# Optimization experiments

Hardware: AMD Instinct MI355X
Metric: run time of the kernel (lower is better)

Reference implementation:

```python
import jax, jax.numpy as jnp
import numpy as np
import math

B, S, D, H = 8, 512, 768, 12
DK = D // H
NEG = 1.0e9


def _split_heads(x):
    # [B,S,D] -> [B,H,S,DK]
    b, s, d = x.shape
    return x.reshape(b, s, H, DK).transpose(0, 2, 1, 3)


def setup_inputs() -> dict:
    key = jax.random.key(0)
    ks = jax.random.split(key, 16)
    std = 1.0 / math.sqrt(D)
    query = jax.random.normal(ks[0], (B, S, D), jnp.float32)
    key_t = jax.random.normal(ks[1], (B, S, D), jnp.float32)
    # mask: 0 for valid tokens, -10000 sentinel for padding
    mask = jnp.where(jax.random.bernoulli(ks[2], 0.9, (B, S)), 0.0, -10000.0).astype(jnp.float32)
    # span targets: binary [H,B,S,S]
    span_matrix = jax.random.bernoulli(ks[3], 0.1, (H, B, S, S)).astype(jnp.float32)
    def lin(i):
        W = jax.random.normal(ks[4 + 2 * i], (D, D), jnp.float32) * std
        b = jax.random.normal(ks[5 + 2 * i], (D,), jnp.float32) * std
        return W, b
    Wql, bql = lin(0)
    Wkl, bkl = lin(1)
    Wqr, bqr = lin(2)
    Wkr, bkr = lin(3)
    Wq, bq = lin(4)
    Wk, bk = lin(5)
    return dict(query=query, key=key_t, mask=mask, span_matrix=span_matrix,
                Wql=Wql, bql=bql, Wkl=Wkl, bkl=bkl,
                Wqr=Wqr, bqr=bqr, Wkr=Wkr, bkr=bkr,
                Wq=Wq, bq=bq, Wk=Wk, bk=bk)


def _forward(query, key, mask, span_matrix,
             Wql, bql, Wkl, bkl, Wqr, bqr, Wkr, bkr, Wq, bq, Wk, bk):
    scale = 1.0 / math.sqrt(D)  # note: original scales by sqrt(model_dim), not sqrt(d_k)
    idx = jnp.arange(S)
    lower = idx[None, :] <= idx[:, None]  # [S,S] lower-triangular incl. diag
    left_boundary = jnp.where(lower, 0.0, NEG)   # 1e9 above diagonal
    right_boundary = left_boundary.T             # 1e9 below diagonal

    # left branch
    ql = _split_heads(query @ Wql + bql) * scale
    kl = _split_heads(key @ Wkl + bkl)
    left_scores = jnp.einsum('bhqd,bhkd->bhqk', ql, kl)
    theta_l = jax.nn.softmax(left_scores - left_boundary, axis=-1)

    # right branch
    qr = _split_heads(query @ Wqr + bqr) * scale
    kr = _split_heads(key @ Wkr + bkr)
    right_scores = jnp.einsum('bhqd,bhkd->bhqk', qr, kr)
    theta_r = jax.nn.softmax(right_scores - right_boundary, axis=-1)

    # theta_l @ upperTri == inclusive cumsum over last axis (O(S) instead of O(S^2) matmul)
    soft_Mask_l = jnp.cumsum(theta_l, axis=-1)
    # theta_r @ lowerTri == inclusive reverse cumsum over last axis
    soft_Mask_r = jnp.cumsum(theta_r[..., ::-1], axis=-1)[..., ::-1]
    soft_Mask = soft_Mask_l * soft_Mask_r

    # main attention
    q = _split_heads(query @ Wq + bq) * scale
    k = _split_heads(key @ Wk + bk)
    att_scores = jnp.einsum('bhqd,bhkd->bhqk', q, k)
    row_mask = jnp.where(mask == -10000.0, NEG, mask)  # [B,S]
    att_scores = att_scores - row_mask[:, None, :, None] - row_mask[:, None, None, :]
    p_local_attn = jax.nn.softmax(att_scores * soft_Mask, axis=-1)

    # per-head BCE between sigmoid(attn) and span targets; mean over heads of per-head means
    # == global mean since every head has the same element count
    span = span_matrix.transpose(1, 0, 2, 3)  # [B,H,S,S]
    p_sig = jax.nn.sigmoid(p_local_attn)      # in (0.5, 0.732], logs are safe
    bce = -(span * jnp.log(p_sig) + (1.0 - span) * jnp.log1p(-p_sig))
    span_loss = jnp.mean(bce)
    return p_local_attn, span_loss


def reference(query, key, mask, span_matrix,
              Wql, bql, Wkl, bkl, Wqr, bqr, Wkr, bkr, Wq, bq, Wk, bk):
    return _forward(query, key, mask, span_matrix,
                    Wql, bql, Wkl, bkl, Wqr, bqr, Wkr, bkr, Wq, bq, Wk, bk)
```

## Files before the change

### kernel.cpp

```cpp
#include <hip/hip_runtime.h>
#include <math.h>

#define BB 8
#define SS 512
#define DD 768
#define HH 12
#define DKK 64
#define NTOK (BB*SS)
#define NELEM (25165824ull)
#define NPROJ 3145728
#define WSZ   589824
#define SCALEQ 0.03608439182435161f

typedef unsigned short u16;
typedef short short8 __attribute__((ext_vector_type(8)));
typedef float f32x4 __attribute__((ext_vector_type(4)));
typedef unsigned short u16x4 __attribute__((ext_vector_type(4)));

#define MFMA16 __builtin_amdgcn_mfma_f32_16x16x32_bf16

__device__ inline u16 f32_to_bf16(float f) {
    unsigned int u = __float_as_uint(f);
    unsigned int r = u + 0x7fffu + ((u >> 16) & 1u);
    return (u16)(r >> 16);
}
__device__ inline float bf16_to_f32(u16 h) {
    return __uint_as_float(((unsigned int)h) << 16);
}

__device__ __forceinline__ void gld16(const u16* g, u16* l) {
    __builtin_amdgcn_global_load_lds(
        (const __attribute__((address_space(1))) unsigned int*)g,
        (__attribute__((address_space(3))) unsigned int*)l, 16, 0, 0);
}

__global__ __launch_bounds__(256)
void cast_wT(const float* __restrict__ W0, const float* __restrict__ W1,
             const float* __restrict__ W2, const float* __restrict__ W3,
             const float* __restrict__ W4, const float* __restrict__ W5,
             u16* __restrict__ WTh, u16* __restrict__ WTl,
             float* __restrict__ lossp)
{
    __shared__ float tile[32][33];
    if (blockIdx.x == 0 && blockIdx.y == 0 && blockIdx.z == 0 && threadIdx.x == 0)
        *lossp = 0.0f;
    const int z = blockIdx.z;
    const float* W;
    switch (z) {
        case 0: W = W0; break; case 1: W = W1; break; case 2: W = W2; break;
        case 3: W = W3; break; case 4: W = W4; break; default: W = W5; break;
    }
    u16* th = WTh + (size_t)z * WSZ;
    u16* tl = WTl + (size_t)z * WSZ;
    const int t = threadIdx.x;
    const int k0 = blockIdx.y * 32, n0 = blockIdx.x * 32;
    const int rr = t >> 3, c0 = (t & 7) * 4;

    float4 v = *(const float4*)(W + (size_t)(k0 + rr) * DD + n0 + c0);
    tile[rr][c0 + 0] = v.x; tile[rr][c0 + 1] = v.y;
    tile[rr][c0 + 2] = v.z; tile[rr][c0 + 3] = v.w;
    __syncthreads();

    u16x4 hw, lw;
#pragma unroll
    for (int i = 0; i < 4; ++i) {
        float f = tile[c0 + i][rr];
        u16 hi = f32_to_bf16(f);
        hw[i] = hi;
        lw[i] = f32_to_bf16(f - bf16_to_f32(hi));
    }
    size_t o = (size_t)(n0 + rr) * DD + k0 + c0;
    *(u16x4*)&th[o] = hw;
    *(u16x4*)&tl[o] = lw;
}

__global__ __launch_bounds__(256)
void cast_X(const float* __restrict__ query, const float* __restrict__ key,
            u16* __restrict__ Xh, u16* __restrict__ Xl)
{
    const float* src = blockIdx.y ? key : query;
    u16* dh = Xh + (size_t)blockIdx.y * NPROJ;
    u16* dl = Xl + (size_t)blockIdx.y * NPROJ;
    size_t i0 = ((size_t)blockIdx.x * 256 + threadIdx.x) * 8;
    float f[8];
    *(float4*)&f[0] = *(const float4*)(src + i0);
    *(float4*)&f[4] = *(const float4*)(src + i0 + 4);
    short8 h, l;
#pragma unroll
    for (int i = 0; i < 8; ++i) {
        u16 hi = f32_to_bf16(f[i]);
        h[i] = (short)hi;
        l[i] = (short)f32_to_bf16(f[i] - bf16_to_f32(hi));
    }
    *(short8*)&dh[i0] = h;
    *(short8*)&dl[i0] = l;
}

__global__ __launch_bounds__(256)
void proj_gemm_gld(const u16* __restrict__ Xh, const u16* __restrict__ Xl,
                   const u16* __restrict__ WTh, const u16* __restrict__ WTl,
                   const float* __restrict__ b0, const float* __restrict__ b1,
                   const float* __restrict__ b2, const float* __restrict__ b3,
                   const float* __restrict__ b4, const float* __restrict__ b5,
                   u16* __restrict__ Ph, u16* __restrict__ Pl)
{
    __shared__ alignas(16) u16 Ash[128][32];
    __shared__ alignas(16) u16 Asl[128][32];
    __shared__ alignas(16) u16 Bsh[128][32];
    __shared__ alignas(16) u16 Bsl[128][32];

    const int z = blockIdx.z;
    const float* bias;
    switch (z) {
        case 0: bias = b0; break; case 1: bias = b1; break; case 2: bias = b2; break;
        case 3: bias = b3; break; case 4: bias = b4; break; default: bias = b5; break;
    }
    const float scl = (z & 1) ? 1.0f : SCALEQ;
    const u16* Ah_g = Xh + (size_t)(z & 1) * NPROJ;
    const u16* Al_g = Xl + (size_t)(z & 1) * NPROJ;
    const u16* WThz = WTh + (size_t)z * WSZ;
    const u16* WTlz = WTl + (size_t)z * WSZ;
    u16* Ch = Ph + (size_t)z * NPROJ;
    u16* Cl = Pl + (size_t)z * NPROJ;
    const bool wlo = (z < 4);

    const int t = threadIdx.x;
    const int w = t >> 6, l = t & 63, quad = l >> 4, ln = l & 15;
    const int m0 = blockIdx.y * 128, n0 = blockIdx.x * 128;
    const int wm = (w & 1) * 64, wn = (w >> 1) * 64;

    const int srow = w * 16 + (l >> 2);
    const int scol = (l & 3) * 8;
    const u16* gAh = Ah_g + (size_t)(m0 + srow) * DD + scol;
    const u16* gAl = Al_g + (size_t)(m0 + srow) * DD + scol;
    const u16* gBh = WThz + (size_t)(n0 + srow) * DD + scol;
    const u16* gBl = WTlz + (size_t)(n0 + srow) * DD + scol;
    u16* lAh0 = &Ash[w * 16][0];      u16* lAh1 = &Ash[w * 16 + 64][0];
    u16* lAl0 = &Asl[w * 16][0];      u16* lAl1 = &Asl[w * 16 + 64][0];
    u16* lBh0 = &Bsh[w * 16][0];      u16* lBh1 = &Bsh[w * 16 + 64][0];
    u16* lBl0 = &Bsl[w * 16][0];      u16* lBl1 = &Bsl[w * 16 + 64][0];
    const size_t rstep = (size_t)64 * DD;

    f32x4 acc[4][4];
#pragma unroll
    for (int i = 0; i < 4; ++i)
#pragma unroll
        for (int jj = 0; jj < 4; ++jj) acc[i][jj] = (f32x4){0.f, 0.f, 0.f, 0.f};

    for (int k0 = 0; k0 < DD; k0 += 32) {
        gld16(gAh + k0, lAh0);  gld16(gAh + k0 + rstep, lAh1);
        gld16(gBh + k0, lBh0);  gld16(gBh + k0 + rstep, lBh1);
        if (wlo) {
            gld16(gAl + k0, lAl0);  gld16(gAl + k0 + rstep, lAl1);
            gld16(gBl + k0, lBl0);  gld16(gBl + k0 + rstep, lBl1);
        }
        __syncthreads();

        short8 afh[4], afl[4], bfh[4], bfl[4];
#pragma unroll
        for (int mt = 0; mt < 4; ++mt)
            afh[mt] = *(const short8*)&Ash[wm + mt * 16 + ln][quad * 8];
#pragma unroll
        for (int nt = 0; nt < 4; ++nt)
            bfh[nt] = *(const short8*)&Bsh[wn + nt * 16 + ln][quad * 8];
        if (wlo) {
#pragma unroll
            for (int mt = 0; mt < 4; ++mt)
                afl[mt] = *(const short8*)&Asl[wm + mt * 16 + ln][quad * 8];
#pragma unroll
            for (int nt = 0; nt < 4; ++nt)
                bfl[nt] = *(const short8*)&Bsl[wn + nt * 16 + ln][quad * 8];
        }
#pragma unroll
        for (int mt = 0; mt < 4; ++mt)
#pragma unroll
            for (int nt = 0; nt < 4; ++nt) {
                acc[mt][nt] = MFMA16(bfh[nt], afh[mt], acc[mt][nt], 0, 0, 0);
                if (wlo) {
                    acc[mt][nt] = MFMA16(bfl[nt], afh[mt], acc[mt][nt], 0, 0, 0);
                    acc[mt][nt] = MFMA16(bfh[nt], afl[mt], acc[mt][nt], 0, 0, 0);
                }
            }
        __syncthreads();
    }

#pragma unroll
    for (int nt = 0; nt < 4; ++nt) {
        const int nb4 = n0 + wn + nt * 16 + quad * 4;
        float4 bias4 = *(const float4*)(bias + nb4);
        float bv[4] = {bias4.x, bias4.y, bias4.z, bias4.w};
#pragma unroll
        for (int mt = 0; mt < 4; ++mt) {
            const int m = m0 + wm + mt * 16 + ln;
            u16x4 hv, lv;
#pragma unroll
            for (int reg = 0; reg < 4; ++reg) {
                float c = (acc[mt][nt][reg] + bv[reg]) * scl;
                u16 hi = f32_to_bf16(c);
                hv[reg] = hi;
                lv[reg] = f32_to_bf16(c - bf16_to_f32(hi));
            }
            size_t o = (size_t)m * DD + nb4;
            *(u16x4*)&Ch[o] = hv;
            if (wlo) *(u16x4*)&Cl[o] = lv;
        }
    }
}

__global__ __launch_bounds__(256)
void proj_gemm_mfma(const float* __restrict__ query, const float* __restrict__ key,
                    const u16* __restrict__ WTh, const u16* __restrict__ WTl,
                    const float* __restrict__ b0, const float* __restrict__ b1,
                    const float* __restrict__ b2, const float* __restrict__ b3,
                    const float* __restrict__ b4, const float* __restrict__ b5,
                    u16* __restrict__ Ph, u16* __restrict__ Pl)
{
    __shared__ alignas(16) u16 Ash[128][40];
    __shared__ alignas(16) u16 Asl[128][40];
    __shared__ alignas(16) u16 Bsh[128][40];
    __shared__ alignas(16) u16 Bsl[128][40];

    const int z = blockIdx.z;
    const float* X = (z & 1) ? key : query;
    const float* bias;
    switch (z) {
        case 0: bias = b0; break; case 1: bias = b1; break; case 2: bias = b2; break;
        case 3: bias = b3; break; case 4: bias = b4; break; default: bias = b5; break;
    }
    const float scl = (z & 1) ? 1.0f : SCALEQ;
    const u16* WThz = WTh + (size_t)z * WSZ;
    const u16* WTlz = WTl + (size_t)z * WSZ;
    u16* Ch = Ph + (size_t)z * NPROJ;
    u16* Cl = Pl + (size_t)z * NPROJ;
    const bool wlo = (z < 4);

    const int t = threadIdx.x;
    const int w = t >> 6, l = t & 63, quad = l >> 4, ln = l & 15;
    const int m0 = blockIdx.y * 128, n0 = blockIdx.x * 128;
    const int wm = (w & 1) * 64, wn = (w >> 1) * 64;

    const int arow = t >> 1, akoff = (t & 1) * 16;
    const int brow = t >> 1, bkoff = (t & 1) * 16;

    f32x4 acc[4][4];
#pragma unroll
    for (int i = 0; i < 4; ++i)
#pragma unroll
        for (int jj = 0; jj < 4; ++jj) acc[i][jj] = (f32x4){0.f, 0.f, 0.f, 0.f};

    for (int k0 = 0; k0 < DD; k0 += 32) {
        {
            const float* asrc = X + (size_t)(m0 + arow) * DD + k0 + akoff;
            float fa[16];
            *(float4*)&fa[0]  = *(const float4*)(asrc + 0);
            *(float4*)&fa[4]  = *(const float4*)(asrc + 4);
            *(float4*)&fa[8]  = *(const float4*)(asrc + 8);
            *(float4*)&fa[12] = *(const float4*)(asrc + 12);
            short8 h0, h1, l0, l1;
#pragma unroll
            for (int i = 0; i < 8; ++i) {
                u16 hi = f32_to_bf16(fa[i]);
                h0[i] = (short)hi;
                l0[i] = (short)f32_to_bf16(fa[i] - bf16_to_f32(hi));
                u16 hi2 = f32_to_bf16(fa[8 + i]);
                h1[i] = (short)hi2;
                l1[i] = (short)f32_to_bf16(fa[8 + i] - bf16_to_f32(hi2));
            }
            *(short8*)&Ash[arow][akoff]     = h0;
            *(short8*)&Ash[arow][akoff + 8] = h1;
            *(short8*)&Asl[arow][akoff]     = l0;
            *(short8*)&Asl[arow][akoff + 8] = l1;
        }
        {
            const u16* bhp = WThz + (size_t)(n0 + brow) * DD + k0 + bkoff;
            const u16* blp = WTlz + (size_t)(n0 + brow) * DD + k0 + bkoff;
            *(uint4*)&Bsh[brow][bkoff]     = *(const uint4*)(bhp);
            *(uint4*)&Bsh[brow][bkoff + 8] = *(const uint4*)(bhp + 8);
            *(uint4*)&Bsl[brow][bkoff]     = *(const uint4*)(blp);
            *(uint4*)&Bsl[brow][bkoff + 8] = *(const uint4*)(blp + 8);
        }
        __syncthreads();

        short8 afh[4], afl[4], bfh[4], bfl[4];
#pragma unroll
        for (int mt = 0; mt < 4; ++mt) {
            afh[mt] = *(const short8*)&Ash[wm + mt * 16 + ln][quad * 8];
            afl[mt] = *(const short8*)&Asl[wm + mt * 16 + ln][quad * 8];
        }
#pragma unroll
        for (int nt = 0; nt < 4; ++nt) {
            bfh[nt] = *(const short8*)&Bsh[wn + nt * 16 + ln][quad * 8];
            bfl[nt] = *(const short8*)&Bsl[wn + nt * 16 + ln][quad * 8];
        }
#pragma unroll
        for (int mt = 0; mt < 4; ++mt)
#pragma unroll
            for (int nt = 0; nt < 4; ++nt) {
                acc[mt][nt] = MFMA16(bfh[nt], afh[mt], acc[mt][nt], 0, 0, 0);
                acc[mt][nt] = MFMA16(bfl[nt], afh[mt], acc[mt][nt], 0, 0, 0);
                acc[mt][nt] = MFMA16(bfh[nt], afl[mt], acc[mt][nt], 0, 0, 0);
            }
        __syncthreads();
    }

#pragma unroll
    for (int nt = 0; nt < 4; ++nt) {
        const int nb4 = n0 + wn + nt * 16 + quad * 4;
        float4 bias4 = *(const float4*)(bias + nb4);
        float bv[4] = {bias4.x, bias4.y, bias4.z, bias4.w};
#pragma unroll
        for (int mt = 0; mt < 4; ++mt) {
            const int m = m0 + wm + mt * 16 + ln;
            u16x4 hv, lv;
#pragma unroll
            for (int reg = 0; reg < 4; ++reg) {
                float c = (acc[mt][nt][reg] + bv[reg]) * scl;
                u16 hi = f32_to_bf16(c);
                hv[reg] = hi;
                lv[reg] = f32_to_bf16(c - bf16_to_f32(hi));
            }
            size_t o = (size_t)m * DD + nb4;
            *(u16x4*)&Ch[o] = hv;
            if (wlo) *(u16x4*)&Cl[o] = lv;
        }
    }
}

#define CHK 128
__global__ __launch_bounds__(512, 4)
void attn_mfma(const u16* __restrict__ Ph, const u16* __restrict__ Pl,
               const float* __restrict__ mask, const float* __restrict__ span,
               float* __restrict__ outp, float* __restrict__ lossp)
{
    __shared__ alignas(16) u16 Kth[CHK][72];
    __shared__ alignas(16) u16 Ktl[CHK][72];
    __shared__ float curb[16][516];
    __shared__ float lred[8];

    const int t = threadIdx.x;
    const int blk = blockIdx.x;
    const int qt = blk & 31;
    const int bh = blk >> 5;
    const int b = bh / HH, h = bh % HH;
    const int w = t >> 6, l = t & 63, quad = l >> 4, ln = l & 15;
    const int r = t >> 5, j = t & 31;
    const int qrow = qt * 16 + r;

    float smbr[16];

    auto compute_scores = [&](const u16* Qh, const u16* Ql,
                              const u16* Kh, const u16* Kl, bool use_lo) {
        const u16* qb = Qh + (size_t)(b * SS + qt * 16 + ln) * DD + h * DKK;
        short8 ah0 = *(const short8*)(qb + quad * 8);
        short8 ah1 = *(const short8*)(qb + 32 + quad * 8);
        short8 al0 = ah0, al1 = ah1;
        if (use_lo) {
            const u16* qb2 = Ql + (size_t)(b * SS + qt * 16 + ln) * DD + h * DKK;
            al0 = *(const short8*)(qb2 + quad * 8);
            al1 = *(const short8*)(qb2 + 32 + quad * 8);
        }
        for (int kc = 0; kc < SS / CHK; ++kc) {
            {
                int row = t >> 2, co = (t & 3) * 16;
                const u16* src = Kh + (size_t)(b * SS + kc * CHK + row) * DD + h * DKK + co;
                *(uint4*)&Kth[row][co]     = *(const uint4*)(src);
                *(uint4*)&Kth[row][co + 8] = *(const uint4*)(src + 8);
                if (use_lo) {
                    const u16* src2 = Kl + (size_t)(b * SS + kc * CHK + row) * DD + h * DKK + co;
                    *(uint4*)&Ktl[row][co]     = *(const uint4*)(src2);
                    *(uint4*)&Ktl[row][co + 8] = *(const uint4*)(src2 + 8);
                }
            }
            __syncthreads();
            const int nb = w * 16;
            short8 bh0 = *(const short8*)&Kth[nb + ln][quad * 8];
            short8 bh1 = *(const short8*)&Kth[nb + ln][32 + quad * 8];
            f32x4 acc = (f32x4){0.f, 0.f, 0.f, 0.f};
            acc = MFMA16(ah0, bh0, acc, 0, 0, 0);
            acc = MFMA16(ah1, bh1, acc, 0, 0, 0);
            if (use_lo) {
                short8 bl0 = *(const short8*)&Ktl[nb + ln][quad * 8];
                short8 bl1 = *(const short8*)&Ktl[nb + ln][32 + quad * 8];
                acc = MFMA16(ah0, bl0, acc, 0, 0, 0);
                acc = MFMA16(ah1, bl1, acc, 0, 0, 0);
                acc = MFMA16(al0, bh0, acc, 0, 0, 0);
                acc = MFMA16(al1, bh1, acc, 0, 0, 0);
            }
            const int cbase = kc * CHK + nb + ln;
#pragma unroll
            for (int reg = 0; reg < 4; ++reg)
                curb[quad * 4 + reg][cbase] = acc[reg];
            __syncthreads();
        }
    };

    compute_scores(Ph + 0 * (size_t)NPROJ, Pl + 0 * (size_t)NPROJ,
                   Ph + 1 * (size_t)NPROJ, Pl + 1 * (size_t)NPROJ, true);
    {
        float e[16];
        float mx = -3.0e38f;
#pragma unroll
        for (int u = 0; u < 16; ++u) {
            int c = u * 32 + j;
            float v = curb[r][c];
            if (c <= qrow && v > mx) mx = v;
        }
#pragma unroll
        for (int off = 16; off >= 1; off >>= 1) mx = fmaxf(mx, __shfl_xor(mx, off));
        float sum = 0.0f;
#pragma unroll
        for (int u = 0; u < 16; ++u) {
            int c = u * 32 + j;
            float v = (c <= qrow) ? __expf(curb[r][c] - mx) : 0.0f;
            e[u] = v; sum += v;
        }
#pragma unroll
        for (int off = 16; off >= 1; off >>= 1) sum += __shfl_xor(sum, off);
        float inv = 1.0f / sum;
        float run = 0.0f;
#pragma unroll
        for (int u = 0; u < 16; ++u) {
            float sc = e[u];
#pragma unroll
            for (int off = 1; off < 32; off <<= 1) {
                float ww = __shfl_up(sc, off, 32);
                if (j >= off) sc += ww;
            }
            smbr[u] = (run + sc) * inv;
            run += __shfl(sc, 31, 32);
        }
    }

    compute_scores(Ph + 2 * (size_t)NPROJ, Pl + 2 * (size_t)NPROJ,
                   Ph + 3 * (size_t)NPROJ, Pl + 3 * (size_t)NPROJ, true);
    {
        float e[16];
        float mx = -3.0e38f;
#pragma unroll
        for (int u = 0; u < 16; ++u) {
            int c = u * 32 + j;
            float v = curb[r][c];
            if (c >= qrow && v > mx) mx = v;
        }
#pragma unroll
        for (int off = 16; off >= 1; off >>= 1) mx = fmaxf(mx, __shfl_xor(mx, off));
        float sum = 0.0f;
#pragma unroll
        for (int u = 0; u < 16; ++u) {
            int c = u * 32 + j;
            float v = (c >= qrow) ? __expf(curb[r][c] - mx) : 0.0f;
            e[u] = v; sum += v;
        }
#pragma unroll
        for (int off = 16; off >= 1; off >>= 1) sum += __shfl_xor(sum, off);
        float inv = 1.0f / sum;
        float run = 0.0f;
#pragma unroll
        for (int u = 15; u >= 0; --u) {
            float sc = e[u];
#pragma unroll
            for (int off = 1; off < 32; off <<= 1) {
                float ww = __shfl_down(sc, off, 32);
                if (j + off < 32) sc += ww;
            }
            smbr[u] *= (run + sc) * inv;
            run += __shfl(sc, 0, 32);
        }
    }

    compute_scores(Ph + 4 * (size_t)NPROJ, (const u16*)0,
                   Ph + 5 * (size_t)NPROJ, (const u16*)0, false);
    {
        float mv  = mask[b * SS + qrow];
        float rmq = (mv == -10000.0f) ? 1.0e9f : mv;
        float vb[16];
        float mx = -3.0e38f;
#pragma unroll
        for (int u = 0; u < 16; ++u) {
            int c = u * 32 + j;
            float mk  = mask[b * SS + c];
            float rmk = (mk == -10000.0f) ? 1.0e9f : mk;
            float v = (curb[r][c] - rmq - rmk) * smbr[u];
            vb[u] = v;
            mx = fmaxf(mx, v);
        }
#pragma unroll
        for (int off = 16; off >= 1; off >>= 1) mx = fmaxf(mx, __shfl_xor(mx, off));
        float sum = 0.0f;
#pragma unroll
        for (int u = 0; u < 16; ++u) {
            float ev = __expf(vb[u] - mx);
            vb[u] = ev; sum += ev;
        }
#pragma unroll
        for (int off = 16; off >= 1; off >>= 1) sum += __shfl_xor(sum, off);
        float inv = 1.0f / sum;

        float* orow = outp + (((size_t)(b * HH + h) * SS + qrow)) * SS;
        const float* sprow = span + (((size_t)(h * BB + b) * SS + qrow)) * SS;
        float lsum = 0.0f;
#pragma unroll
        for (int u = 0; u < 16; ++u) {
            int c = u * 32 + j;
            float p = vb[u] * inv;
            orow[c] = p;
            float s = sprow[c];
            lsum += __logf(1.0f + __expf(-p)) + (1.0f - s) * p;
        }
#pragma unroll
        for (int off = 32; off >= 1; off >>= 1) lsum += __shfl_xor(lsum, off);
        if ((t & 63) == 0) lred[t >> 6] = lsum;
        __syncthreads();
        if (t == 0) {
            float tot = 0.0f;
#pragma unroll
            for (int i = 0; i < 8; ++i) tot += lred[i];
            atomicAdd(lossp, tot * (float)(1.0 / 25165824.0));
        }
    }
}

extern "C" void kernel_launch(void* const* d_in, const int* in_sizes, int n_in,
                              void* d_out, int out_size, void* d_ws, size_t ws_size,
                              hipStream_t stream)
{
    const float* query = (const float*)d_in[0];
    const float* key_t = (const float*)d_in[1];
    const float* mask  = (const float*)d_in[2];
    const float* span  = (const float*)d_in[3];
    const float* Wql = (const float*)d_in[4];  const float* bql = (const float*)d_in[5];
    const float* Wkl = (const float*)d_in[6];  const float* bkl = (const float*)d_in[7];
    const float* Wqr = (const float*)d_in[8];  const float* bqr = (const float*)d_in[9];
    const float* Wkr = (const float*)d_in[10]; const float* bkr = (const float*)d_in[11];
    const float* Wq  = (const float*)d_in[12]; const float* bq  = (const float*)d_in[13];
    const float* Wk  = (const float*)d_in[14]; const float* bk  = (const float*)d_in[15];

    float* out = (float*)d_out;
    float* lossp = out + NELEM;

    u16* ws16 = (u16*)d_ws;
    u16* WTh = ws16;
    u16* WTl = WTh + (size_t)6 * WSZ;
    u16* Ph  = WTl + (size_t)6 * WSZ;
    u16* Pl  = Ph + (size_t)6 * NPROJ;
    u16* Xh  = Pl + (size_t)4 * NPROJ;
    u16* Xl  = Xh + (size_t)2 * NPROJ;
    const size_t need_big = ((size_t)12 * WSZ + (size_t)14 * NPROJ) * 2;
    const bool bigws = ws_size >= need_big;

    cast_wT<<<dim3(24, 24, 6), dim3(256), 0, stream>>>(
        Wql, Wkl, Wqr, Wkr, Wq, Wk, WTh, WTl, lossp);

    if (bigws) {
        cast_X<<<dim3(1536, 2), dim3(256), 0, stream>>>(query, key_t, Xh, Xl);
        proj_gemm_gld<<<dim3(DD / 128, NTOK / 128, 6), dim3(256), 0, stream>>>(
            Xh, Xl, WTh, WTl, bql, bkl, bqr, bkr, bq, bk, Ph, Pl);
    } else {
        proj_gemm_mfma<<<dim3(DD / 128, NTOK / 128, 6), dim3(256), 0, stream>>>(
            query, key_t, WTh, WTl, bql, bkl, bqr, bkr, bq, bk, Ph, Pl);
    }

    attn_mfma<<<dim3(96 * 32), dim3(512), 0, stream>>>(
        Ph, Pl, mask, span, out, lossp);
}
```

Baseline: 455.6 us.

## Load K fragments directly from global memory, drop LDS staging and per-chunk barriers

The score computation now reads the K operands for each MFMA straight from global memory into registers, removing the Kth/Ktl LDS tiles and the two __syncthreads per chunk. That cuts LDS use and allows a higher occupancy hint in launch bounds (8 blocks instead of 4). The softmax cumsum was also restructured: the separate sum reduction is dropped and the total is taken from the running scan, and the 16 independent warp scans are unrolled together for more ILP. The cost is more uncoalesced global or L2 traffic for K, and more register pressure from the 16-wide scan under the tighter launch bound.

```diff
diff --git a/kernel.cpp b/kernel.cpp
--- a/kernel.cpp
+++ b/kernel.cpp
@@ -326,14 +326,11 @@
     }
 }
 
-#define CHK 128
-__global__ __launch_bounds__(512, 4)
+__global__ __launch_bounds__(512, 8)
 void attn_mfma(const u16* __restrict__ Ph, const u16* __restrict__ Pl,
                const float* __restrict__ mask, const float* __restrict__ span,
                float* __restrict__ outp, float* __restrict__ lossp)
 {
-    __shared__ alignas(16) u16 Kth[CHK][72];
-    __shared__ alignas(16) u16 Ktl[CHK][72];
     __shared__ float curb[16][516];
     __shared__ float lred[8];
 
@@ -350,122 +347,116 @@
 
     auto compute_scores = [&](const u16* Qh, const u16* Ql,
                               const u16* Kh, const u16* Kl, bool use_lo) {
-        const u16* qb = Qh + (size_t)(b * SS + qt * 16 + ln) * DD + h * DKK;
-        short8 ah0 = *(const short8*)(qb + quad * 8);
-        short8 ah1 = *(const short8*)(qb + 32 + quad * 8);
+        const size_t qoff = (size_t)(b * SS + qt * 16 + ln) * DD + h * DKK + quad * 8;
+        short8 ah0 = *(const short8*)(Qh + qoff);
+        short8 ah1 = *(const short8*)(Qh + qoff + 32);
         short8 al0 = ah0, al1 = ah1;
         if (use_lo) {
-            const u16* qb2 = Ql + (size_t)(b * SS + qt * 16 + ln) * DD + h * DKK;
-            al0 = *(const short8*)(qb2 + quad * 8);
-            al1 = *(const short8*)(qb2 + 32 + quad * 8);
-        }
-        for (int kc = 0; kc < SS / CHK; ++kc) {
-            {
-                int row = t >> 2, co = (t & 3) * 16;
-                const u16* src = Kh + (size_t)(b * SS + kc * CHK + row) * DD + h * DKK + co;
-                *(uint4*)&Kth[row][co]     = *(const uint4*)(src);
-                *(uint4*)&Kth[row][co + 8] = *(const uint4*)(src + 8);
-                if (use_lo) {
-                    const u16* src2 = Kl + (size_t)(b * SS + kc * CHK + row) * DD + h * DKK + co;
-                    *(uint4*)&Ktl[row][co]     = *(const uint4*)(src2);
-                    *(uint4*)&Ktl[row][co + 8] = *(const uint4*)(src2 + 8);
-                }
-            }
-            __syncthreads();
-            const int nb = w * 16;
-            short8 bh0 = *(const short8*)&Kth[nb + ln][quad * 8];
-            short8 bh1 = *(const short8*)&Kth[nb + ln][32 + quad * 8];
+            al0 = *(const short8*)(Ql + qoff);
+            al1 = *(const short8*)(Ql + qoff + 32);
+        }
+        const size_t koff = (size_t)(b * SS + w * 16 + ln) * DD + h * DKK + quad * 8;
+        const u16* kb = Kh + koff;
+        const u16* klb = use_lo ? (Kl + koff) : kb;
+        __syncthreads();
+#pragma unroll
+        for (int kc = 0; kc < 4; ++kc) {
+            const size_t off = (size_t)kc * (128 * DD);
+            short8 bh0 = *(const short8*)(kb + off);
+            short8 bh1 = *(const short8*)(kb + off + 32);
             f32x4 acc = (f32x4){0.f, 0.f, 0.f, 0.f};
             acc = MFMA16(ah0, bh0, acc, 0, 0, 0);
             acc = MFMA16(ah1, bh1, acc, 0, 0, 0);
             if (use_lo) {
-                short8 bl0 = *(const short8*)&Ktl[nb + ln][quad * 8];
-                short8 bl1 = *(const short8*)&Ktl[nb + ln][32 + quad * 8];
+                short8 bl0 = *(const short8*)(klb + off);
+                short8 bl1 = *(const short8*)(klb + off + 32);
                 acc = MFMA16(ah0, bl0, acc, 0, 0, 0);
                 acc = MFMA16(ah1, bl1, acc, 0, 0, 0);
                 acc = MFMA16(al0, bh0, acc, 0, 0, 0);
                 acc = MFMA16(al1, bh1, acc, 0, 0, 0);
             }
-            const int cbase = kc * CHK + nb + ln;
+            const int cbase = kc * 128 + w * 16 + ln;
 #pragma unroll
             for (int reg = 0; reg < 4; ++reg)
                 curb[quad * 4 + reg][cbase] = acc[reg];
-            __syncthreads();
-        }
+        }
+        __syncthreads();
     };
 
     compute_scores(Ph + 0 * (size_t)NPROJ, Pl + 0 * (size_t)NPROJ,
                    Ph + 1 * (size_t)NPROJ, Pl + 1 * (size_t)NPROJ, true);
     {
-        float e[16];
+        float sc[16];
         float mx = -3.0e38f;
 #pragma unroll
         for (int u = 0; u < 16; ++u) {
             int c = u * 32 + j;
             float v = curb[r][c];
+            sc[u] = v;
             if (c <= qrow && v > mx) mx = v;
         }
 #pragma unroll
         for (int off = 16; off >= 1; off >>= 1) mx = fmaxf(mx, __shfl_xor(mx, off));
-        float sum = 0.0f;
 #pragma unroll
         for (int u = 0; u < 16; ++u) {
             int c = u * 32 + j;
-            float v = (c <= qrow) ? __expf(curb[r][c] - mx) : 0.0f;
-            e[u] = v; sum += v;
-        }
-#pragma unroll
-        for (int off = 16; off >= 1; off >>= 1) sum += __shfl_xor(sum, off);
-        float inv = 1.0f / sum;
+            sc[u] = (c <= qrow) ? __expf(sc[u] - mx) : 0.0f;
+        }
+#pragma unroll
+        for (int u = 0; u < 16; ++u) {
+#pragma unroll
+            for (int off = 1; off < 32; off <<= 1) {
+                float ww = __shfl_up(sc[u], off, 32);
+                if (j >= off) sc[u] += ww;
+            }
+        }
         float run = 0.0f;
 #pragma unroll
         for (int u = 0; u < 16; ++u) {
-            float sc = e[u];
-#pragma unroll
-            for (int off = 1; off < 32; off <<= 1) {
-                float ww = __shfl_up(sc, off, 32);
-                if (j >= off) sc += ww;
-            }
-            smbr[u] = (run + sc) * inv;
-            run += __shfl(sc, 31, 32);
-        }
+            smbr[u] = run + sc[u];
+            run += __shfl(sc[u], 31, 32);
+        }
+        float inv = 1.0f / run;
+#pragma unroll
+        for (int u = 0; u < 16; ++u) smbr[u] *= inv;
     }
 
     compute_scores(Ph + 2 * (size_t)NPROJ, Pl + 2 * (size_t)NPROJ,
                    Ph + 3 * (size_t)NPROJ, Pl + 3 * (size_t)NPROJ, true);
     {
-        float e[16];
+        float sc[16];
         float mx = -3.0e38f;
 #pragma unroll
         for (int u = 0; u < 16; ++u) {
             int c = u * 32 + j;
             float v = curb[r][c];
+            sc[u] = v;
             if (c >= qrow && v > mx) mx = v;
         }
 #pragma unroll
         for (int off = 16; off >= 1; off >>= 1) mx = fmaxf(mx, __shfl_xor(mx, off));
-        float sum = 0.0f;
 #pragma unroll
         for (int u = 0; u < 16; ++u) {
             int c = u * 32 + j;
-            float v = (c >= qrow) ? __expf(curb[r][c] - mx) : 0.0f;
-            e[u] = v; sum += v;
-        }
-#pragma unroll
-        for (int off = 16; off >= 1; off >>= 1) sum += __shfl_xor(sum, off);
-        float inv = 1.0f / sum;
+            sc[u] = (c >= qrow) ? __expf(sc[u] - mx) : 0.0f;
+        }
+#pragma unroll
+        for (int u = 0; u < 16; ++u) {
+#pragma unroll
+            for (int off = 1; off < 32; off <<= 1) {
+                float ww = __shfl_down(sc[u], off, 32);
+                if (j + off < 32) sc[u] += ww;
+            }
+        }
         float run = 0.0f;
 #pragma unroll
         for (int u = 15; u >= 0; --u) {
-            float sc = e[u];
-#pragma unroll
-            for (int off = 1; off < 32; off <<= 1) {
-                float ww = __shfl_down(sc, off, 32);
-                if (j + off < 32) sc += ww;
-            }
-            smbr[u] *= (run + sc) * inv;
-            run += __shfl(sc, 0, 32);
-        }
+            smbr[u] *= (run + sc[u]);
+            run += __shfl(sc[u], 0, 32);
+        }
+        float inv = 1.0f / run;
+#pragma unroll
+        for (int u = 0; u < 16; ++u) smbr[u] *= inv;
     }
 
     compute_scores(Ph + 4 * (size_t)NPROJ, (const u16*)0,
```

After: 518.1 us. 1.14x slower.
